# Kernel optimization log

Hardware: AMD Instinct MI355X
Metric: run time of the kernel (lower is better)

## Reference

```python
import jax, jax.numpy as jnp
import numpy as np

B, C, Q, D = 64, 1024, 256, 128
NEG = -1e30  # VERY_NEGATIVE_NUMBER


def setup_inputs() -> dict:
    key = jax.random.key(0)
    k1, k2, k3, k4, k5, k6 = jax.random.split(key, 6)
    return {
        "x_cont": jax.random.normal(k1, (B, C, D), dtype=jnp.float32),
        "x_ques": jax.random.normal(k2, (B, Q, D), dtype=jnp.float32),
        "c_mask": jnp.ones((B, C), dtype=jnp.float32),
        "q_mask": jnp.ones((B, Q), dtype=jnp.float32),
        "W0": jax.random.uniform(k3, (D, 1), jnp.float32, -0.1, 0.1),
        "W1": jax.random.uniform(k4, (D, 1), jnp.float32, -0.1, 0.1),
        "W2": jax.random.uniform(k5, (1, 1, D), jnp.float32, -0.1, 0.1),
        "bias": jnp.zeros((1,), dtype=jnp.float32),
    }


def reference(x_cont, x_ques, c_mask, q_mask, W0, W1, W2, bias):
    # Trilinear similarity S[b,c,q] = x_cont.W0 + x_ques.W1 + (x_cont*W2).x_ques^T + bias
    s0 = x_cont @ W0                                   # [B,C,1]
    s1 = jnp.swapaxes(x_ques @ W1, 1, 2)               # [B,1,Q]
    s2 = jnp.einsum('bcd,bqd->bcq', x_cont * W2, x_ques)  # [B,C,Q]
    S = s0 + s1 + s2 + bias                            # [B,C,Q]

    qm = q_mask[:, None, :]                            # [B,1,Q]
    cm = c_mask[:, :, None]                            # [B,C,1]
    S_ = jax.nn.softmax(S + NEG * (1.0 - qm), axis=-1)           # row softmax [B,C,Q]
    S_T = jnp.swapaxes(jax.nn.softmax(S + NEG * (1.0 - cm), axis=1), 1, 2)  # [B,Q,C]

    c2q = S_ @ x_ques                                  # [B,C,D]
    q2c = (S_ @ S_T) @ x_cont                          # [B,C,D]
    return jnp.concatenate([x_cont, c2q, x_cont * c2q, x_cont * q2c], axis=-1)
```

## Files before the change

### kernel.cpp

```cpp
#include <hip/hip_runtime.h>
#include <math.h>

#define BB 64
#define CC 1024
#define QQ 256
#define DD 128
#define NEGV (-1.0e30f)

typedef short bf8 __attribute__((ext_vector_type(8)));
typedef short bf4 __attribute__((ext_vector_type(4)));
typedef float f4v __attribute__((ext_vector_type(4)));

__device__ __forceinline__ short f2bf(float f) {
    unsigned u = __builtin_bit_cast(unsigned, f);
    u += 0x7FFFu + ((u >> 16) & 1u);
    return (short)(u >> 16);
}
__device__ __forceinline__ float bf2f(short s) {
    unsigned u = ((unsigned)(unsigned short)s) << 16;
    return __builtin_bit_cast(float, u);
}

__global__ __launch_bounds__(256, 4) void k0_all(
        const float* __restrict__ xc, const float* __restrict__ xq,
        const float* __restrict__ W0, const float* __restrict__ W1,
        const float* __restrict__ W2,
        const float* __restrict__ c_mask, const float* __restrict__ q_mask,
        float* __restrict__ s0m, float* __restrict__ s1m,
        short* __restrict__ xc_bf, short* __restrict__ xqw_bf,
        short* __restrict__ xcT_bf, short* __restrict__ xqT_bf) {
    __shared__ float tile[64][129];
    int bid = blockIdx.x;
    const float *src, *W, *mask;
    float* sm; short *rm, *tr;
    int b, tl, R; bool use2;
    if (bid < 1024) {
        b = ((bid >> 7) << 3) | (bid & 7); tl = (bid >> 3) & 15; R = CC;
        src = xc; W = W0; mask = c_mask; sm = s0m; rm = xc_bf; tr = xcT_bf; use2 = false;
    } else {
        int q = bid - 1024;
        b = ((q >> 5) << 3) | (q & 7); tl = (q >> 3) & 3; R = QQ;
        src = xq; W = W1; mask = q_mask; sm = s1m; rm = xqw_bf; tr = xqT_bf; use2 = true;
    }
    int r0 = tl * 64;
    int t = threadIdx.x;
    int c4 = t & 31, rr = t >> 5;
    float4 wv = ((const float4*)W)[c4];
    float4 sc4 = use2 ? ((const float4*)W2)[c4] : make_float4(1.f, 1.f, 1.f, 1.f);
    const float* sb = src + ((size_t)b * R + r0) * DD;
    #pragma unroll
    for (int p = 0; p < 8; ++p) {
        int row = rr + p * 8;
        float4 g = *(const float4*)&sb[(size_t)row * DD + c4 * 4];
        bf4 o;
        o[0] = f2bf(g.x * sc4.x); o[1] = f2bf(g.y * sc4.y);
        o[2] = f2bf(g.z * sc4.z); o[3] = f2bf(g.w * sc4.w);
        *(bf4*)&rm[((size_t)(b * R + r0 + row)) * DD + c4 * 4] = o;
        float part = g.x * wv.x + g.y * wv.y + g.z * wv.z + g.w * wv.w;
        #pragma unroll
        for (int off = 1; off < 32; off <<= 1) part += __shfl_xor(part, off, 64);
        if ((t & 31) == 0)
            sm[(size_t)b * R + r0 + row] =
                part + NEGV * (1.0f - mask[(size_t)b * R + r0 + row]);
        tile[row][c4 * 4 + 0] = g.x; tile[row][c4 * 4 + 1] = g.y;
        tile[row][c4 * 4 + 2] = g.z; tile[row][c4 * 4 + 3] = g.w;
    }
    __syncthreads();
    int rj = (t & 7) * 8;
    #pragma unroll
    for (int pp = 0; pp < 4; ++pp) {
        int d = pp * 32 + (t >> 3);
        bf8 o;
        #pragma unroll
        for (int j = 0; j < 8; ++j) o[j] = f2bf(tile[rj + j][d]);
        *(bf8*)&tr[((size_t)(b * DD + d)) * R + r0 + rj] = o;
    }
}

#define SCP 1032
#define S2P 264
#define XTP 72

#define K1_LDA(G, S, CT)                                                 \
    {                                                                    \
        const short* ar_ = abase + (size_t)(CT) * 64 * DD;               \
        G[0] = *(const bf8*)&ar_[0];  G[1] = *(const bf8*)&ar_[32];      \
        G[2] = *(const bf8*)&ar_[64]; G[3] = *(const bf8*)&ar_[96];      \
        S = *(const f4v*)&s0base[(CT) * 64];                             \
    }

#define K1_STEPA(G, S, CT)                                                            \
    {                                                                                 \
        f4v acc = {0.f, 0.f, 0.f, 0.f};                                               \
        acc = __builtin_amdgcn_mfma_f32_16x16x32_bf16(G[0], bq[0], acc, 0, 0, 0);     \
        acc = __builtin_amdgcn_mfma_f32_16x16x32_bf16(G[1], bq[1], acc, 0, 0, 0);     \
        acc = __builtin_amdgcn_mfma_f32_16x16x32_bf16(G[2], bq[2], acc, 0, 0, 0);     \
        acc = __builtin_amdgcn_mfma_f32_16x16x32_bf16(G[3], bq[3], acc, 0, 0, 0);     \
        bf4 ov;                                                                       \
        ov[0] = f2bf(acc[0] + S[0]); ov[1] = f2bf(acc[1] + S[1]);                     \
        ov[2] = f2bf(acc[2] + S[2]); ov[3] = f2bf(acc[3] + S[3]);                     \
        *(bf4*)&sc[l16][(CT) * 64 + w * 16 + quad * 4] = ov;                          \
        if ((CT) + 4 < 16) K1_LDA(G, S, (CT) + 4);                                    \
    }

#define K1_LDS2(G, CT)                                                   \
    {                                                                    \
        G[0] = *(const bf8*)&tbase[(CT) * 64];                           \
        G[1] = *(const bf8*)&tbase[(size_t)8 * CC + (CT) * 64];          \
        G[2] = *(const bf8*)&tbase[(size_t)16 * CC + (CT) * 64];         \
        G[3] = *(const bf8*)&tbase[(size_t)24 * CC + (CT) * 64];         \
    }

#define K1_WRS2(G)                                                       \
    {                                                                    \
        *(bf8*)&xct[w][sr][c8l * 8] = G[0];                              \
        *(bf8*)&xct[w][sr + 8][c8l * 8] = G[1];                          \
        *(bf8*)&xct[w][sr + 16][c8l * 8] = G[2];                         \
        *(bf8*)&xct[w][sr + 24][c8l * 8] = G[3];                         \
    }

#define K1_CSTEP(CT)                                                               \
    {                                                                              \
        bf8 a0 = *(const bf8*)&sc[l16][(CT) * 64 + quad * 8];                      \
        bf8 b0 = *(const bf8*)&xct[w][l16][quad * 8];                              \
        acc0 = __builtin_amdgcn_mfma_f32_16x16x32_bf16(a0, b0, acc0, 0, 0, 0);     \
        bf8 b1 = *(const bf8*)&xct[w][16 + l16][quad * 8];                         \
        acc1 = __builtin_amdgcn_mfma_f32_16x16x32_bf16(a0, b1, acc1, 0, 0, 0);     \
        bf8 a1 = *(const bf8*)&sc[l16][(CT) * 64 + 32 + quad * 8];                 \
        bf8 b2 = *(const bf8*)&xct[w][l16][32 + quad * 8];                         \
        acc0 = __builtin_amdgcn_mfma_f32_16x16x32_bf16(a1, b2, acc0, 0, 0, 0);     \
        bf8 b3 = *(const bf8*)&xct[w][16 + l16][32 + quad * 8];                    \
        acc1 = __builtin_amdgcn_mfma_f32_16x16x32_bf16(a1, b3, acc1, 0, 0, 0);     \
    }

#define K1_ROT(G, CT)                                                    \
    {                                                                    \
        K1_WRS2(G);                                                      \
        if ((CT) + 4 < 16) K1_LDS2(G, (CT) + 4);                         \
    }

__global__ __launch_bounds__(256, 3) void k1_colsm(
        const short* __restrict__ xc_bf, const short* __restrict__ xcT_bf,
        const short* __restrict__ xqw_bf, const float* __restrict__ s0m,
        short* __restrict__ AT) {
    __shared__ __align__(16) short sc[16][SCP];
    __shared__ __align__(16) short xct[4][32][XTP];
    __shared__ float invl[16];

    int bid = blockIdx.x;
    int qt = (bid >> 3) & 15;
    int b = ((bid >> 7) << 3) | (bid & 7);
    int q0 = qt * 16;
    int t = threadIdx.x, w = t >> 6, l = t & 63;
    int quad = l >> 4, l16 = l & 15;

    bf8 bq[4];
    {
        const short* qp = &xqw_bf[(size_t)(b * QQ + q0 + l16) * DD + quad * 8];
        #pragma unroll
        for (int ks = 0; ks < 4; ++ks) bq[ks] = *(const bf8*)&qp[ks * 32];
    }

    const short* abase = &xc_bf[(size_t)(b * CC + w * 16 + l16) * DD + quad * 8];
    const float* s0base = &s0m[b * CC + w * 16 + quad * 4];
    bf8 gA[4], gB[4], gC[4], gD[4];
    f4v sA, sB, sC, sD;
    K1_LDA(gA, sA, 0); K1_LDA(gB, sB, 1); K1_LDA(gC, sC, 2); K1_LDA(gD, sD, 3);
    #pragma unroll
    for (int c4t = 0; c4t < 16; c4t += 4) {
        K1_STEPA(gA, sA, c4t + 0);
        K1_STEPA(gB, sB, c4t + 1);
        K1_STEPA(gC, sC, c4t + 2);
        K1_STEPA(gD, sD, c4t + 3);
    }

    int c8l = l & 7, sr = l >> 3;
    const short* tbase = &xcT_bf[(size_t)(b * DD + w * 32 + sr) * CC + c8l * 8];
    bf8 gS0[4], gS1[4], gS2[4];
    K1_LDS2(gS0, 0);
    K1_LDS2(gS1, 1);
    K1_LDS2(gS2, 2);

    __syncthreads();

    {
        int q = t >> 4, k = t & 15;
        bf8 v[8];
        #pragma unroll
        for (int j = 0; j < 8; ++j) v[j] = *(const bf8*)&sc[q][k * 8 + j * 128];
        float m = -3.0e38f;
        #pragma unroll
        for (int j = 0; j < 8; ++j)
            #pragma unroll
            for (int e = 0; e < 8; ++e) m = fmaxf(m, bf2f(v[j][e]));
        #pragma unroll
        for (int off = 1; off < 16; off <<= 1) m = fmaxf(m, __shfl_xor(m, off, 64));
        float sum = 0.f;
        #pragma unroll
        for (int j = 0; j < 8; ++j) {
            bf8 o;
            #pragma unroll
            for (int e = 0; e < 8; ++e) {
                float ex = __expf(bf2f(v[j][e]) - m);
                sum += ex;
                o[e] = f2bf(ex);
            }
            *(bf8*)&sc[q][k * 8 + j * 128] = o;
        }
        #pragma unroll
        for (int off = 1; off < 16; off <<= 1) sum += __shfl_xor(sum, off, 64);
        if (k == 0) invl[q] = 1.0f / sum;
    }
    __syncthreads();

    f4v acc0 = {0.f, 0.f, 0.f, 0.f}, acc1 = {0.f, 0.f, 0.f, 0.f};
    K1_WRS2(gS0);
    K1_LDS2(gS0, 3);
    #pragma unroll
    for (int ct = 0; ct < 16; ++ct) {
        K1_CSTEP(ct);
        if (ct < 15) {
            int nb = (ct + 1) % 3;
            if (nb == 0)      K1_ROT(gS0, ct)
            else if (nb == 1) K1_ROT(gS1, ct)
            else              K1_ROT(gS2, ct)
        }
    }
    {
        bf4 o0, o1;
        #pragma unroll
        for (int r = 0; r < 4; ++r) {
            float il = invl[quad * 4 + r];
            o0[r] = f2bf(acc0[r] * il);
            o1[r] = f2bf(acc1[r] * il);
        }
        int d0 = w * 32 + l16;
        *(bf4*)&AT[(size_t)(b * DD + d0) * QQ + q0 + quad * 4] = o0;
        *(bf4*)&AT[(size_t)(b * DD + d0 + 16) * QQ + q0 + quad * 4] = o1;
    }
}

#define K2_LDA(G, CT)                                                    \
    {                                                                    \
        const short* ar_ = abase + (size_t)(CT) * 64 * DD;               \
        G[0] = *(const bf8*)&ar_[0];  G[1] = *(const bf8*)&ar_[32];      \
        G[2] = *(const bf8*)&ar_[64]; G[3] = *(const bf8*)&ar_[96];      \
    }

#define K2_STEP1(G, SV, QT)                                                           \
    {                                                                                 \
        f4v acc0 = {0.f, 0.f, 0.f, 0.f}, acc1 = {0.f, 0.f, 0.f, 0.f};                 \
        acc0 = __builtin_amdgcn_mfma_f32_16x16x32_bf16(G[0], bc0[0], acc0, 0, 0, 0);  \
        acc1 = __builtin_amdgcn_mfma_f32_16x16x32_bf16(G[0], bc1[0], acc1, 0, 0, 0);  \
        acc0 = __builtin_amdgcn_mfma_f32_16x16x32_bf16(G[1], bc0[1], acc0, 0, 0, 0);  \
        acc1 = __builtin_amdgcn_mfma_f32_16x16x32_bf16(G[1], bc1[1], acc1, 0, 0, 0);  \
        acc0 = __builtin_amdgcn_mfma_f32_16x16x32_bf16(G[2], bc0[2], acc0, 0, 0, 0);  \
        acc1 = __builtin_amdgcn_mfma_f32_16x16x32_bf16(G[2], bc1[2], acc1, 0, 0, 0);  \
        acc0 = __builtin_amdgcn_mfma_f32_16x16x32_bf16(G[3], bc0[3], acc0, 0, 0, 0);  \
        acc1 = __builtin_amdgcn_mfma_f32_16x16x32_bf16(G[3], bc1[3], acc1, 0, 0, 0);  \
        int qbase_ = (QT) * 64 + w * 16 + quad * 4;                                   \
        bf4 o0, o1;                                                                   \
        o0[0] = f2bf(acc0[0] + SV[0]); o0[1] = f2bf(acc0[1] + SV[1]);                 \
        o0[2] = f2bf(acc0[2] + SV[2]); o0[3] = f2bf(acc0[3] + SV[3]);                 \
        o1[0] = f2bf(acc1[0] + SV[0]); o1[1] = f2bf(acc1[1] + SV[1]);                 \
        o1[2] = f2bf(acc1[2] + SV[2]); o1[3] = f2bf(acc1[3] + SV[3]);                 \
        *(bf4*)&sc2[l16][qbase_] = o0;                                                \
        *(bf4*)&sc2[16 + l16][qbase_] = o1;                                           \
    }

#define K2_SRC(NT) ((NT) < 4 ? (qtb + (size_t)((NT) & 3) * 64) : (atb + (size_t)((NT) - 4) * 64))

#define K2_LDS2(G, NT)                                                   \
    {                                                                    \
        const short* gs_ = K2_SRC(NT);                                   \
        G[0] = *(const bf8*)&gs_[0];                                     \
        G[1] = *(const bf8*)&gs_[(size_t)8 * QQ];                        \
        G[2] = *(const bf8*)&gs_[(size_t)16 * QQ];                       \
        G[3] = *(const bf8*)&gs_[(size_t)24 * QQ];                       \
    }

#define K2_WRS2(G)                                                       \
    {                                                                    \
        *(bf8*)&tT[w][sr][c8l * 8] = G[0];                               \
        *(bf8*)&tT[w][sr + 8][c8l * 8] = G[1];                           \
        *(bf8*)&tT[w][sr + 16][c8l * 8] = G[2];                          \
        *(bf8*)&tT[w][sr + 24][c8l * 8] = G[3];                          \
    }

#define K2_CSTEP(TL)                                                                   \
    {                                                                                  \
        int qoff_ = ((TL) & 3) * 64;                                                   \
        _Pragma("unroll")                                                              \
        for (int ks = 0; ks < 2; ++ks) {                                               \
            bf8 a0 = *(const bf8*)&sc2[l16][qoff_ + ks * 32 + quad * 8];               \
            bf8 a1 = *(const bf8*)&sc2[16 + l16][qoff_ + ks * 32 + quad * 8];          \
            bf8 b0 = *(const bf8*)&tT[w][l16][ks * 32 + quad * 8];                     \
            bf8 b1 = *(const bf8*)&tT[w][16 + l16][ks * 32 + quad * 8];                \
            if ((TL) < 4) {                                                            \
                ac[0][0] = __builtin_amdgcn_mfma_f32_16x16x32_bf16(a0, b0, ac[0][0], 0, 0, 0); \
                ac[0][1] = __builtin_amdgcn_mfma_f32_16x16x32_bf16(a0, b1, ac[0][1], 0, 0, 0); \
                ac[1][0] = __builtin_amdgcn_mfma_f32_16x16x32_bf16(a1, b0, ac[1][0], 0, 0, 0); \
                ac[1][1] = __builtin_amdgcn_mfma_f32_16x16x32_bf16(a1, b1, ac[1][1], 0, 0, 0); \
            } else {                                                                   \
                aq[0][0] = __builtin_amdgcn_mfma_f32_16x16x32_bf16(a0, b0, aq[0][0], 0, 0, 0); \
                aq[0][1] = __builtin_amdgcn_mfma_f32_16x16x32_bf16(a0, b1, aq[0][1], 0, 0, 0); \
                aq[1][0] = __builtin_amdgcn_mfma_f32_16x16x32_bf16(a1, b0, aq[1][0], 0, 0, 0); \
                aq[1][1] = __builtin_amdgcn_mfma_f32_16x16x32_bf16(a1, b1, aq[1][1], 0, 0, 0); \
            }                                                                          \
        }                                                                              \
    }

#define K2_ROT(G, TL)                                                    \
    {                                                                    \
        K2_WRS2(G);                                                      \
        if ((TL) + 4 < 8) K2_LDS2(G, (TL) + 4);                          \
    }

__global__ __launch_bounds__(256, 4) void k2_rowsm(
        const float* __restrict__ xc, const short* __restrict__ xc_bf,
        const short* __restrict__ xqw_bf, const short* __restrict__ xqT_bf,
        const short* __restrict__ AT, const float* __restrict__ s1m,
        float* __restrict__ out) {
    __shared__ __align__(16) short sc2[32][S2P];
    __shared__ __align__(16) short tT[4][32][XTP];
    __shared__ float invl2[32];

    int bid = blockIdx.x;
    int cb = (bid >> 3) & 31;
    int b = ((bid >> 8) << 3) | (bid & 7);
    int c0g = cb * 32;
    int t = threadIdx.x, w = t >> 6, l = t & 63;
    int quad = l >> 4, l16 = l & 15;

    bf8 bc0[4], bc1[4];
    {
        const short* p0 = &xc_bf[(size_t)(b * CC + c0g + l16) * DD + quad * 8];
        const short* p1 = p0 + 16 * DD;
        #pragma unroll
        for (int ks = 0; ks < 4; ++ks) {
            bc0[ks] = *(const bf8*)&p0[ks * 32];
            bc1[ks] = *(const bf8*)&p1[ks * 32];
        }
    }

    const short* abase = &xqw_bf[(size_t)(b * QQ + w * 16 + l16) * DD + quad * 8];
    const float* s1base = &s1m[b * QQ + w * 16 + quad * 4];
    f4v sv0 = *(const f4v*)&s1base[0];
    f4v sv1 = *(const f4v*)&s1base[64];
    f4v sv2 = *(const f4v*)&s1base[128];
    f4v sv3 = *(const f4v*)&s1base[192];
    bf8 gA[4], gB[4];
    K2_LDA(gA, 0); K2_LDA(gB, 1);
    K2_STEP1(gA, sv0, 0); K2_LDA(gA, 2);
    K2_STEP1(gB, sv1, 1); K2_LDA(gB, 3);
    K2_STEP1(gA, sv2, 2);
    K2_STEP1(gB, sv3, 3);

    int c8l = l & 7, sr = l >> 3;
    const short* qtb = &xqT_bf[(size_t)(b * DD + w * 32 + sr) * QQ + c8l * 8];
    const short* atb = &AT[(size_t)(b * DD + w * 32 + sr) * QQ + c8l * 8];
    bf8 gS0[4], gS1[4], gS2[4];
    K2_LDS2(gS0, 0);
    K2_LDS2(gS1, 1);
    K2_LDS2(gS2, 2);

    __syncthreads();

    {
        int c = t >> 3, k = t & 7;
        bf8 v[4];
        #pragma unroll
        for (int j = 0; j < 4; ++j) v[j] = *(const bf8*)&sc2[c][k * 8 + j * 64];
        float m = -3.0e38f;
        #pragma unroll
        for (int j = 0; j < 4; ++j)
            #pragma unroll
            for (int e = 0; e < 8; ++e) m = fmaxf(m, bf2f(v[j][e]));
        #pragma unroll
        for (int off = 1; off < 8; off <<= 1) m = fmaxf(m, __shfl_xor(m, off, 64));
        float sum = 0.f;
        #pragma unroll
        for (int j = 0; j < 4; ++j) {
            bf8 o;
            #pragma unroll
            for (int e = 0; e < 8; ++e) {
                float ex = __expf(bf2f(v[j][e]) - m);
                sum += ex;
                o[e] = f2bf(ex);
            }
            *(bf8*)&sc2[c][k * 8 + j * 64] = o;
        }
        #pragma unroll
        for (int off = 1; off < 8; off <<= 1) sum += __shfl_xor(sum, off, 64);
        if (k == 0) invl2[c] = 1.0f / sum;
    }
    __syncthreads();

    f4v ac[2][2], aq[2][2];
    f4v zz = {0.f, 0.f, 0.f, 0.f};
    #pragma unroll
    for (int i = 0; i < 2; ++i)
        #pragma unroll
        for (int j = 0; j < 2; ++j) { ac[i][j] = zz; aq[i][j] = zz; }
    K2_WRS2(gS0);
    K2_LDS2(gS0, 3);
    #pragma unroll
    for (int tl = 0; tl < 8; ++tl) {
        K2_CSTEP(tl);
        if (tl < 7) {
            int nb = (tl + 1) % 3;
            if (nb == 0)      K2_ROT(gS0, tl)
            else if (nb == 1) K2_ROT(gS1, tl)
            else              K2_ROT(gS2, tl)
        }
    }

    __syncthreads();
    float (*c2l)[132] = (float(*)[132])sc2;
    float (*q2l)[132] = (float(*)[132])tT;
    #pragma unroll
    for (int cf = 0; cf < 2; ++cf)
        #pragma unroll
        for (int df = 0; df < 2; ++df)
            #pragma unroll
            for (int r = 0; r < 4; ++r) {
                int cl = cf * 16 + quad * 4 + r;
                int d = w * 32 + df * 16 + l16;
                c2l[cl][d] = ac[cf][df][r];
                q2l[cl][d] = aq[cf][df][r];
            }
    __syncthreads();
    {
        int cl = t >> 3, j4 = (t & 7) * 4;
        float il = invl2[cl];
        const float* xrow = xc + (size_t)(b * CC + c0g + cl) * DD;
        float* orow = out + (size_t)(b * CC + c0g + cl) * (4 * DD);
        #pragma unroll
        for (int ps = 0; ps < 4; ++ps) {
            int d = ps * 32 + j4;
            float4 xv = *(const float4*)&xrow[d];
            float4 cv = *(const float4*)&c2l[cl][d];
            float4 qv = *(const float4*)&q2l[cl][d];
            cv.x *= il; cv.y *= il; cv.z *= il; cv.w *= il;
            qv.x *= il; qv.y *= il; qv.z *= il; qv.w *= il;
            *(float4*)&orow[d] = xv;
            *(float4*)&orow[DD + d] = cv;
            float4 m2 = make_float4(xv.x * cv.x, xv.y * cv.y, xv.z * cv.z, xv.w * cv.w);
            *(float4*)&orow[2 * DD + d] = m2;
            float4 m3 = make_float4(xv.x * qv.x, xv.y * qv.y, xv.z * qv.z, xv.w * qv.w);
            *(float4*)&orow[3 * DD + d] = m3;
        }
    }
}

extern "C" void kernel_launch(void* const* d_in, const int* in_sizes, int n_in,
                              void* d_out, int out_size, void* d_ws, size_t ws_size,
                              hipStream_t stream) {
    const float* x_cont = (const float*)d_in[0];
    const float* x_ques = (const float*)d_in[1];
    const float* c_mask = (const float*)d_in[2];
    const float* q_mask = (const float*)d_in[3];
    const float* W0     = (const float*)d_in[4];
    const float* W1     = (const float*)d_in[5];
    const float* W2     = (const float*)d_in[6];
    float* out = (float*)d_out;

    char* ws = (char*)d_ws;
    float* s0m    = (float*)ws;  ws += (size_t)BB * CC * 4;
    float* s1m    = (float*)ws;  ws += (size_t)BB * QQ * 4;
    short* xc_bf  = (short*)ws;  ws += (size_t)BB * CC * DD * 2;
    short* xqw_bf = (short*)ws;  ws += (size_t)BB * QQ * DD * 2;
    short* xcT_bf = (short*)ws;  ws += (size_t)BB * CC * DD * 2;
    short* xqT_bf = (short*)ws;  ws += (size_t)BB * QQ * DD * 2;
    short* AT     = (short*)ws;

    k0_all<<<BB * 16 + BB * 4, 256, 0, stream>>>(x_cont, x_ques, W0, W1, W2,
                                                 c_mask, q_mask, s0m, s1m,
                                                 xc_bf, xqw_bf, xcT_bf, xqT_bf);
    k1_colsm<<<BB * 16, 256, 0, stream>>>(xc_bf, xcT_bf, xqw_bf, s0m, AT);
    k2_rowsm<<<BB * 32, 256, 0, stream>>>(x_cont, xc_bf, xqw_bf, xqT_bf, AT, s1m, out);
}
```

Baseline: 259.0 us.

## Double k1 block to 512 threads and store k0 transpose tile as bf16

```diff
diff --git a/kernel.cpp b/kernel.cpp
--- a/kernel.cpp
+++ b/kernel.cpp
@@ -21,7 +21,7 @@
     return __builtin_bit_cast(float, u);
 }
 
-__global__ __launch_bounds__(256, 4) void k0_all(
+__global__ __launch_bounds__(256, 5) void k0_all(
         const float* __restrict__ xc, const float* __restrict__ xq,
         const float* __restrict__ W0, const float* __restrict__ W1,
         const float* __restrict__ W2,
@@ -29,7 +29,7 @@
         float* __restrict__ s0m, float* __restrict__ s1m,
         short* __restrict__ xc_bf, short* __restrict__ xqw_bf,
         short* __restrict__ xcT_bf, short* __restrict__ xqT_bf) {
-    __shared__ float tile[64][129];
+    __shared__ short tile[64][132];
     int bid = blockIdx.x;
     const float *src, *W, *mask;
     float* sm; short *rm, *tr;
@@ -62,8 +62,9 @@
         if ((t & 31) == 0)
             sm[(size_t)b * R + r0 + row] =
                 part + NEGV * (1.0f - mask[(size_t)b * R + r0 + row]);
-        tile[row][c4 * 4 + 0] = g.x; tile[row][c4 * 4 + 1] = g.y;
-        tile[row][c4 * 4 + 2] = g.z; tile[row][c4 * 4 + 3] = g.w;
+        bf4 u;
+        u[0] = f2bf(g.x); u[1] = f2bf(g.y); u[2] = f2bf(g.z); u[3] = f2bf(g.w);
+        *(bf4*)&tile[row][c4 * 4] = u;
     }
     __syncthreads();
     int rj = (t & 7) * 8;
@@ -72,7 +73,7 @@
         int d = pp * 32 + (t >> 3);
         bf8 o;
         #pragma unroll
-        for (int j = 0; j < 8; ++j) o[j] = f2bf(tile[rj + j][d]);
+        for (int j = 0; j < 8; ++j) o[j] = tile[rj + j][d];
         *(bf8*)&tr[((size_t)(b * DD + d)) * R + r0 + rj] = o;
     }
 }
@@ -83,10 +84,10 @@
 
 #define K1_LDA(G, S, CT)                                                 \
     {                                                                    \
-        const short* ar_ = abase + (size_t)(CT) * 64 * DD;               \
+        const short* ar_ = abase + (size_t)(CT) * 128 * DD;              \
         G[0] = *(const bf8*)&ar_[0];  G[1] = *(const bf8*)&ar_[32];      \
         G[2] = *(const bf8*)&ar_[64]; G[3] = *(const bf8*)&ar_[96];      \
-        S = *(const f4v*)&s0base[(CT) * 64];                             \
+        S = *(const f4v*)&s0base[(CT) * 128];                            \
     }
 
 #define K1_STEPA(G, S, CT)                                                            \
@@ -99,24 +100,20 @@
         bf4 ov;                                                                       \
         ov[0] = f2bf(acc[0] + S[0]); ov[1] = f2bf(acc[1] + S[1]);                     \
         ov[2] = f2bf(acc[2] + S[2]); ov[3] = f2bf(acc[3] + S[3]);                     \
-        *(bf4*)&sc[l16][(CT) * 64 + w * 16 + quad * 4] = ov;                          \
-        if ((CT) + 4 < 16) K1_LDA(G, S, (CT) + 4);                                    \
+        *(bf4*)&sc[l16][(CT) * 128 + w * 16 + quad * 4] = ov;                         \
+        if ((CT) + 3 < 8) K1_LDA(G, S, (CT) + 3);                                     \
     }
 
 #define K1_LDS2(G, CT)                                                   \
     {                                                                    \
         G[0] = *(const bf8*)&tbase[(CT) * 64];                           \
         G[1] = *(const bf8*)&tbase[(size_t)8 * CC + (CT) * 64];          \
-        G[2] = *(const bf8*)&tbase[(size_t)16 * CC + (CT) * 64];         \
-        G[3] = *(const bf8*)&tbase[(size_t)24 * CC + (CT) * 64];         \
     }
 
 #define K1_WRS2(G)                                                       \
     {                                                                    \
         *(bf8*)&xct[w][sr][c8l * 8] = G[0];                              \
         *(bf8*)&xct[w][sr + 8][c8l * 8] = G[1];                          \
-        *(bf8*)&xct[w][sr + 16][c8l * 8] = G[2];                         \
-        *(bf8*)&xct[w][sr + 24][c8l * 8] = G[3];                         \
     }
 
 #define K1_CSTEP(CT)                                                               \
@@ -124,13 +121,9 @@
         bf8 a0 = *(const bf8*)&sc[l16][(CT) * 64 + quad * 8];                      \
         bf8 b0 = *(const bf8*)&xct[w][l16][quad * 8];                              \
         acc0 = __builtin_amdgcn_mfma_f32_16x16x32_bf16(a0, b0, acc0, 0, 0, 0);     \
-        bf8 b1 = *(const bf8*)&xct[w][16 + l16][quad * 8];                         \
-        acc1 = __builtin_amdgcn_mfma_f32_16x16x32_bf16(a0, b1, acc1, 0, 0, 0);     \
         bf8 a1 = *(const bf8*)&sc[l16][(CT) * 64 + 32 + quad * 8];                 \
-        bf8 b2 = *(const bf8*)&xct[w][l16][32 + quad * 8];                         \
-        acc0 = __builtin_amdgcn_mfma_f32_16x16x32_bf16(a1, b2, acc0, 0, 0, 0);     \
-        bf8 b3 = *(const bf8*)&xct[w][16 + l16][32 + quad * 8];                    \
-        acc1 = __builtin_amdgcn_mfma_f32_16x16x32_bf16(a1, b3, acc1, 0, 0, 0);     \
+        bf8 b1 = *(const bf8*)&xct[w][l16][32 + quad * 8];                         \
+        acc0 = __builtin_amdgcn_mfma_f32_16x16x32_bf16(a1, b1, acc0, 0, 0, 0);     \
     }
 
 #define K1_ROT(G, CT)                                                    \
@@ -139,12 +132,12 @@
         if ((CT) + 4 < 16) K1_LDS2(G, (CT) + 4);                         \
     }
 
-__global__ __launch_bounds__(256, 3) void k1_colsm(
+__global__ __launch_bounds__(512, 4) void k1_colsm(
         const short* __restrict__ xc_bf, const short* __restrict__ xcT_bf,
         const short* __restrict__ xqw_bf, const float* __restrict__ s0m,
         short* __restrict__ AT) {
     __shared__ __align__(16) short sc[16][SCP];
-    __shared__ __align__(16) short xct[4][32][XTP];
+    __shared__ __align__(16) short xct[8][16][XTP];
     __shared__ float invl[16];
 
     int bid = blockIdx.x;
@@ -163,20 +156,21 @@
 
     const short* abase = &xc_bf[(size_t)(b * CC + w * 16 + l16) * DD + quad * 8];
     const float* s0base = &s0m[b * CC + w * 16 + quad * 4];
-    bf8 gA[4], gB[4], gC[4], gD[4];
-    f4v sA, sB, sC, sD;
-    K1_LDA(gA, sA, 0); K1_LDA(gB, sB, 1); K1_LDA(gC, sC, 2); K1_LDA(gD, sD, 3);
-    #pragma unroll
-    for (int c4t = 0; c4t < 16; c4t += 4) {
-        K1_STEPA(gA, sA, c4t + 0);
-        K1_STEPA(gB, sB, c4t + 1);
-        K1_STEPA(gC, sC, c4t + 2);
-        K1_STEPA(gD, sD, c4t + 3);
-    }
+    bf8 gA[4], gB[4], gC[4];
+    f4v sA, sB, sC;
+    K1_LDA(gA, sA, 0); K1_LDA(gB, sB, 1); K1_LDA(gC, sC, 2);
+    K1_STEPA(gA, sA, 0);
+    K1_STEPA(gB, sB, 1);
+    K1_STEPA(gC, sC, 2);
+    K1_STEPA(gA, sA, 3);
+    K1_STEPA(gB, sB, 4);
+    K1_STEPA(gC, sC, 5);
+    K1_STEPA(gA, sA, 6);
+    K1_STEPA(gB, sB, 7);
 
     int c8l = l & 7, sr = l >> 3;
-    const short* tbase = &xcT_bf[(size_t)(b * DD + w * 32 + sr) * CC + c8l * 8];
-    bf8 gS0[4], gS1[4], gS2[4];
+    const short* tbase = &xcT_bf[(size_t)(b * DD + w * 16 + sr) * CC + c8l * 8];
+    bf8 gS0[2], gS1[2], gS2[2];
     K1_LDS2(gS0, 0);
     K1_LDS2(gS1, 1);
     K1_LDS2(gS2, 2);
@@ -184,20 +178,20 @@
     __syncthreads();
 
     {
-        int q = t >> 4, k = t & 15;
-        bf8 v[8];
-        #pragma unroll
-        for (int j = 0; j < 8; ++j) v[j] = *(const bf8*)&sc[q][k * 8 + j * 128];
+        int q = t >> 5, k = t & 31;
+        bf8 v[4];
+        #pragma unroll
+        for (int j = 0; j < 4; ++j) v[j] = *(const bf8*)&sc[q][k * 8 + j * 256];
         float m = -3.0e38f;
         #pragma unroll
-        for (int j = 0; j < 8; ++j)
+        for (int j = 0; j < 4; ++j)
             #pragma unroll
             for (int e = 0; e < 8; ++e) m = fmaxf(m, bf2f(v[j][e]));
         #pragma unroll
-        for (int off = 1; off < 16; off <<= 1) m = fmaxf(m, __shfl_xor(m, off, 64));
+        for (int off = 1; off < 32; off <<= 1) m = fmaxf(m, __shfl_xor(m, off, 64));
         float sum = 0.f;
         #pragma unroll
-        for (int j = 0; j < 8; ++j) {
+        for (int j = 0; j < 4; ++j) {
             bf8 o;
             #pragma unroll
             for (int e = 0; e < 8; ++e) {
@@ -205,15 +199,15 @@
                 sum += ex;
                 o[e] = f2bf(ex);
             }
-            *(bf8*)&sc[q][k * 8 + j * 128] = o;
-        }
-        #pragma unroll
-        for (int off = 1; off < 16; off <<= 1) sum += __shfl_xor(sum, off, 64);
+            *(bf8*)&sc[q][k * 8 + j * 256] = o;
+        }
+        #pragma unroll
+        for (int off = 1; off < 32; off <<= 1) sum += __shfl_xor(sum, off, 64);
         if (k == 0) invl[q] = 1.0f / sum;
     }
     __syncthreads();
 
-    f4v acc0 = {0.f, 0.f, 0.f, 0.f}, acc1 = {0.f, 0.f, 0.f, 0.f};
+    f4v acc0 = {0.f, 0.f, 0.f, 0.f};
     K1_WRS2(gS0);
     K1_LDS2(gS0, 3);
     #pragma unroll
@@ -227,16 +221,11 @@
         }
     }
     {
-        bf4 o0, o1;
-        #pragma unroll
-        for (int r = 0; r < 4; ++r) {
-            float il = invl[quad * 4 + r];
-            o0[r] = f2bf(acc0[r] * il);
-            o1[r] = f2bf(acc1[r] * il);
-        }
-        int d0 = w * 32 + l16;
+        bf4 o0;
+        #pragma unroll
+        for (int r = 0; r < 4; ++r) o0[r] = f2bf(acc0[r] * invl[quad * 4 + r]);
+        int d0 = w * 16 + l16;
         *(bf4*)&AT[(size_t)(b * DD + d0) * QQ + q0 + quad * 4] = o0;
-        *(bf4*)&AT[(size_t)(b * DD + d0 + 16) * QQ + q0 + quad * 4] = o1;
     }
 }
 
@@ -477,6 +466,6 @@
     k0_all<<<BB * 16 + BB * 4, 256, 0, stream>>>(x_cont, x_ques, W0, W1, W2,
                                                  c_mask, q_mask, s0m, s1m,
                                                  xc_bf, xqw_bf, xcT_bf, xqT_bf);
-    k1_colsm<<<BB * 16, 256, 0, stream>>>(xc_bf, xcT_bf, xqw_bf, s0m, AT);
+    k1_colsm<<<BB * 16, 512, 0, stream>>>(xc_bf, xcT_bf, xqw_bf, s0m, AT);
     k2_rowsm<<<BB * 32, 256, 0, stream>>>(x_cont, xc_bf, xqw_bf, xqT_bf, AT, s1m, out);
 }
```

Result: faster. 252.9 us (-2.4%).
